# Kernel optimization log

Hardware: AMD Instinct MI355X
Metric: run time of the kernel (lower is better)

## Reference

```python
import jax, jax.numpy as jnp
import numpy as np

B, L, D, H = 2, 256, 128, 256


def silu_bwd(x):
    # NOTE: replicates the module's silu_backward exactly: silu(x) + sigmoid(x)*(1 - silu(x))
    s = jax.nn.silu(x)
    return s + jax.nn.sigmoid(x) * (1.0 - s)


def setup_inputs() -> dict:
    key = jax.random.key(0)
    ks = jax.random.split(key, 10)
    f32 = jnp.float32
    return {
        "x": jax.random.normal(ks[0], (B, L, D), f32),
        "W1_init": jax.random.normal(ks[1], (H, D), f32) * H ** -0.5,
        "b1_init": jnp.zeros((H,), f32),
        "W2_init": jax.random.normal(ks[2], (D, H), f32) * D ** -0.5,
        "b2_init": jnp.zeros((D,), f32),
        "Wq": jax.random.normal(ks[3], (D, D), f32) * D ** -0.5,
        "bq": jnp.zeros((D,), f32),
        "Wk": jax.random.normal(ks[4], (D, D), f32) * D ** -0.5,
        "bk": jnp.zeros((D,), f32),
        "Wv": jax.random.normal(ks[5], (D, D), f32) * D ** -0.5,
        "bv": jnp.zeros((D,), f32),
        "Wlr": jax.random.normal(ks[6], (1, D), f32) * D ** -0.5,
        "blr": jnp.zeros((1,), f32),
        "Wm": jax.random.normal(ks[7], (1, D), f32) * D ** -0.5,
        "bm": jnp.zeros((1,), f32),
        "Wwd": jax.random.normal(ks[8], (1, D), f32) * D ** -0.5,
        "bwd": jnp.zeros((1,), f32),
    }


def _forward(x, W1_init, b1_init, W2_init, b2_init, Wq, bq, Wk, bk, Wv, bv,
             Wlr, blr, Wm, bm, Wwd, bwd):
    b, l, d = x.shape
    q = x @ Wq.T + bq
    k = x @ Wk.T + bk
    v = x @ Wv.T + bv

    # fast-weight forward pass with initial weights (first call: state = init params)
    Z1 = jnp.einsum('hd,bld->blh', W1_init, k) + b1_init
    X2 = jax.nn.silu(Z1)
    Z2 = jnp.einsum('dh,blh->bld', W2_init, X2) + b2_init

    # per-token gradients of 0.5*||Z2 - v||^2
    gZ2 = Z2 - v
    gW2 = jnp.einsum('bld,blh->bldh', gZ2, X2)
    gX2 = jnp.einsum('bld,dh->blh', gZ2, W2_init)
    gZ1 = gX2 * silu_bwd(Z1)
    gW1 = jnp.einsum('blh,bld->blhd', gZ1, k)

    lr = jax.nn.softplus(x @ Wlr.T + blr)[..., 0]  # (b,l)
    gW1 = gW1 * lr[:, :, None, None]
    gb1 = gZ1 * lr[:, :, None]
    gW2 = gW2 * lr[:, :, None, None]
    gb2 = gZ2 * lr[:, :, None]

    strict = jnp.tril(jnp.ones((l, l), x.dtype), -1)  # row > col
    incl = jnp.tril(jnp.ones((l, l), x.dtype))        # row >= col

    # momentum: masked log-cumsum trick; [b,l,m] decay matrix
    log_mom = -jax.nn.softplus(-(x @ Wm.T + bm))[..., 0]  # (b,l)
    mom_cs = jnp.exp(jnp.cumsum(log_mom[:, :, None] * strict, axis=1)) * incl
    mW1 = jnp.einsum('blm,bmhd->blhd', mom_cs, gW1)
    mb1 = jnp.einsum('blm,bmh->blh', mom_cs, gb1)
    mW2 = jnp.einsum('blm,bmdh->bldh', mom_cs, gW2)
    mb2 = jnp.einsum('blm,bmd->bld', mom_cs, gb2)
    # cross-chunk momentum terms vanish (momentum state initialized to zero)

    # weight decay gating
    log_wd = -jax.nn.softplus(-(x @ Wwd.T + bwd))[..., 0]
    wd_cs = jnp.exp(jnp.cumsum(log_wd[:, :, None] * strict, axis=1)) * incl
    wd_full = jnp.exp(jnp.cumsum(log_wd, axis=1))  # (b,l)

    W1p = jnp.einsum('blm,bmhd->blhd', wd_cs, mW1) + wd_full[:, :, None, None] * W1_init
    b1p = jnp.einsum('blm,bmh->blh', wd_cs, mb1) + wd_full[:, :, None] * b1_init
    W2p = jnp.einsum('blm,bmdh->bldh', wd_cs, mW2) + wd_full[:, :, None, None] * W2_init
    b2p = jnp.einsum('blm,bmd->bld', wd_cs, mb2) + wd_full[:, :, None] * b2_init

    # query the per-token updated fast weights
    Zq1 = jnp.einsum('blhd,bld->blh', W1p, q) + b1p
    Xq2 = jax.nn.silu(Zq1)
    Zq2 = jnp.einsum('bldh,blh->bld', W2p, Xq2) + b2p
    return Zq2


def reference(x, W1_init, b1_init, W2_init, b2_init, Wq, bq, Wk, bk, Wv, bv,
              Wlr, blr, Wm, bm, Wwd, bwd):
    return _forward(x, W1_init, b1_init, W2_init, b2_init, Wq, bq, Wk, bk, Wv, bv,
                    Wlr, blr, Wm, bm, Wwd, bwd)
```

## Files before the change

### kernel.cpp

```cpp
#include <hip/hip_runtime.h>
#include <hip/hip_bf16.h>


#define Bc 2
#define Lc 256
#define Dc 128
#define Hc 256

__device__ __forceinline__ float sigf(float z)  { return 1.f / (1.f + expf(-z)); }
__device__ __forceinline__ float siluf(float z) { return z * sigf(z); }
__device__ __forceinline__ float silubwdf(float z) {
    float sg = sigf(z);
    float s  = z * sg;
    return s + sg * (1.f - s);
}
__device__ __forceinline__ float softplusf(float z) {
    if (z > 20.f)  return z;
    if (z < -20.f) return expf(z);
    return log1pf(expf(z));
}
__device__ __forceinline__ float dot4(float4 a, float4 b) {
    return a.x*b.x + a.y*b.y + a.z*b.z + a.w*b.w;
}

__global__ __launch_bounds__(256) void k_pre(
    const float* __restrict__ Wq, const float* __restrict__ Wk,
    const float* __restrict__ Wv, const float* __restrict__ W1,
    const float* __restrict__ W2,
    float4* __restrict__ Wq4, float4* __restrict__ Wk4, float4* __restrict__ Wv4,
    float4* __restrict__ W14, float4* __restrict__ W2q4, float4* __restrict__ W2c4)
{
    const int bb = blockIdx.x;
    if (bb < 112) {
        const float* in; float4* o; int M, N, base;
        if      (bb < 16) { in = Wq; o = Wq4;  M = 128; N = 128; base = 0;  }
        else if (bb < 32) { in = Wk; o = Wk4;  M = 128; N = 128; base = 16; }
        else if (bb < 48) { in = Wv; o = Wv4;  M = 128; N = 128; base = 32; }
        else if (bb < 80) { in = W1; o = W14;  M = 256; N = 128; base = 48; }
        else              { in = W2; o = W2q4; M = 128; N = 256; base = 80; }
        const int idx = (bb - base) * 256 + threadIdx.x;
        const int r = idx % M, g = idx / M;
        o[idx] = *(const float4*)(in + r * N + 4 * g);
    } else {
        const int idx = (bb - 112) * 256 + threadIdx.x;
        const int c = idx & 255, g = idx >> 8;
        W2c4[idx] = make_float4(W2[(4*g+0)*Hc + c], W2[(4*g+1)*Hc + c],
                                W2[(4*g+2)*Hc + c], W2[(4*g+3)*Hc + c]);
    }
}

__global__ __launch_bounds__(512, 4) void k_token(
    const float* __restrict__ x,
    const float* __restrict__ b1v, const float* __restrict__ b2v,
    const float* __restrict__ bq,  const float* __restrict__ bk,
    const float* __restrict__ bv,
    const float4* __restrict__ Wq4, const float4* __restrict__ Wk4,
    const float4* __restrict__ Wv4, const float4* __restrict__ W14,
    const float4* __restrict__ W2q4, const float4* __restrict__ W2c4,
    const float* __restrict__ Wlr, const float* __restrict__ blr,
    const float* __restrict__ Wm,  const float* __restrict__ bm,
    const float* __restrict__ Wwd, const float* __restrict__ bwd,
    float* __restrict__ qo, float* __restrict__ KT, float* __restrict__ X2T,
    float* __restrict__ z1q, float* __restrict__ GZ1, float* __restrict__ GZ2,
    float* __restrict__ Ssc, float* __restrict__ wdf)
{
    const int bb  = blockIdx.x;
    const int tid = threadIdx.x;

    if (bb >= Bc * Lc / 2) {
        __shared__ __align__(16) float lrS[Lc];
        __shared__ __align__(16) float lwS[Lc];
        __shared__ __align__(16) float ewdS[Lc];
        __shared__ __align__(16) float clmS[Lc];
        __shared__ __align__(16) float cwdS[Lc];
        const int b = bb - Bc * Lc / 2;
        const int l = tid;
        if (l < Lc) {
            const float4* xr4 = (const float4*)(x + (b * Lc + l) * Dc);
            const float4* wl4 = (const float4*)Wlr;
            const float4* wm4 = (const float4*)Wm;
            const float4* ww4 = (const float4*)Wwd;
            float dlr = blr[0], dm = bm[0], dw = bwd[0];
            #pragma unroll 4
            for (int j = 0; j < Dc / 4; ++j) {
                float4 xv = xr4[j];
                dlr += dot4(wl4[j], xv);
                dm  += dot4(wm4[j], xv);
                dw  += dot4(ww4[j], xv);
            }
            lrS[l] = softplusf(dlr);
            float lm = -softplusf(-dm);
            float lw = -softplusf(-dw);
            lwS[l]  = lw;
            clmS[l] = lm;
            cwdS[l] = lw;
        }
        __syncthreads();
        for (int off = 1; off < Lc; off <<= 1) {
            float a = 0.f, c = 0.f;
            if (l < Lc && l >= off) { a = clmS[l - off]; c = cwdS[l - off]; }
            __syncthreads();
            if (l < Lc) { clmS[l] += a; cwdS[l] += c; }
            __syncthreads();
        }
        if (l < Lc) {
            wdf[b * Lc + l] = expf(cwdS[l]);
            ewdS[l] = __expf(lwS[l]);
        }
        __syncthreads();
        if (l < Lc) {
            const int   m     = l;
            const float clm_m = clmS[m];
            const float lrm   = lrS[m];
            float* outp = Ssc + (b * Lc) * Lc + m;
            const int ll0 = m & ~63;
            {
                int zs = m - 3 < 0 ? 0 : m - 3;
                for (int ll = zs; ll < ll0; ++ll) outp[ll * Lc] = 0.f;
            }
            float s = 0.f;
            for (int ll4 = ll0; ll4 < Lc; ll4 += 8) {
                float4 cla = *(const float4*)&clmS[ll4];
                float4 clb = *(const float4*)&clmS[ll4 + 4];
                float4 ewa = *(const float4*)&ewdS[ll4];
                float4 ewb = *(const float4*)&ewdS[ll4 + 4];
                float ew[8] = {ewa.x, ewa.y, ewa.z, ewa.w,
                               ewb.x, ewb.y, ewb.z, ewb.w};
                float e2[8];
                e2[0] = __expf(cla.x - clm_m); e2[1] = __expf(cla.y - clm_m);
                e2[2] = __expf(cla.z - clm_m); e2[3] = __expf(cla.w - clm_m);
                e2[4] = __expf(clb.x - clm_m); e2[5] = __expf(clb.y - clm_m);
                e2[6] = __expf(clb.z - clm_m); e2[7] = __expf(clb.w - clm_m);
                #pragma unroll
                for (int u = 0; u < 8; ++u) {
                    const int ll = ll4 + u;
                    s = (ll >= m) ? (ew[u] * s + e2[u]) : 0.f;
                    outp[ll * Lc] = s * lrm;
                }
            }
        }
        return;
    }

    __shared__ __align__(16) float xs[2][Dc], qs[2][Dc], ks[2][Dc];
    __shared__ __align__(16) float X2s[2][Hc], z1s[2][Hc], gZ2s[2][Dc];
    __shared__ __align__(16) float pv[2][2][Dc], pz[4][2][Dc], pg[2][2][Hc];

    const int t0 = bb * 2;
    const int b  = t0 >> 8;
    const int l0 = t0 & 255;

    if (tid < 2 * Dc / 4)
        ((float4*)&xs[0][0])[tid] = ((const float4*)(x + t0 * Dc))[tid];
    __syncthreads();

    {
        const int g = tid >> 7, c = tid & 127;
        float4 wb[16];
        if (g < 2) {
            const float4* W = g ? Wk4 : Wq4;
            float a0 = (g ? bk : bq)[c], a1 = a0;
            for (int j4 = 0; j4 < 32; j4 += 16) {
                #pragma unroll
                for (int u = 0; u < 16; ++u) wb[u] = W[(j4+u) * Dc + c];
                #pragma unroll
                for (int u = 0; u < 16; ++u) {
                    a0 += dot4(wb[u], *(const float4*)&xs[0][4*(j4+u)]);
                    a1 += dot4(wb[u], *(const float4*)&xs[1][4*(j4+u)]);
                }
            }
            if (g == 0) {
                qs[0][c] = a0; qs[1][c] = a1;
                qo[t0 * Dc + c] = a0;
                qo[(t0 + 1) * Dc + c] = a1;
            } else {
                ks[0][c] = a0; ks[1][c] = a1;
                float* ktp = KT + (size_t)b * 32768;
                ktp[((c >> 2) * Lc + l0 + 0) * 4 + (c & 3)] = a0;
                ktp[((c >> 2) * Lc + l0 + 1) * 4 + (c & 3)] = a1;
            }
        } else {
            const int half = g - 2, j0 = half * 16;
            float av0 = 0.f, av1 = 0.f;
            #pragma unroll
            for (int u = 0; u < 16; ++u) wb[u] = Wv4[(j0+u) * Dc + c];
            #pragma unroll
            for (int u = 0; u < 16; ++u) {
                av0 += dot4(wb[u], *(const float4*)&xs[0][4*(j0+u)]);
                av1 += dot4(wb[u], *(const float4*)&xs[1][4*(j0+u)]);
            }
            pv[half][0][c] = av0; pv[half][1][c] = av1;
        }
    }
    __syncthreads();

    {
        const int which = tid >> 8, h = tid & 255;
        const float (*src)[Dc] = which ? qs : ks;
        float a0 = b1v[h], a1 = a0;
        float4 wb[16];
        for (int d4 = 0; d4 < 32; d4 += 16) {
            #pragma unroll
            for (int u = 0; u < 16; ++u) wb[u] = W14[(d4+u) * Hc + h];
            #pragma unroll
            for (int u = 0; u < 16; ++u) {
                a0 += dot4(wb[u], *(const float4*)&src[0][4*(d4+u)]);
                a1 += dot4(wb[u], *(const float4*)&src[1][4*(d4+u)]);
            }
        }
        if (which == 0) {
            z1s[0][h] = a0; z1s[1][h] = a1;
            float s0 = siluf(a0), s1 = siluf(a1);
            X2s[0][h] = s0; X2s[1][h] = s1;
            float* xtp = X2T + (size_t)b * 65536;
            xtp[((h >> 2) * Lc + l0 + 0) * 4 + (h & 3)] = s0;
            xtp[((h >> 2) * Lc + l0 + 1) * 4 + (h & 3)] = s1;
        } else {
            z1q[(t0 + 0) * Hc + h] = a0;
            z1q[(t0 + 1) * Hc + h] = a1;
        }
    }
    __syncthreads();

    {
        const int q4g = tid >> 7, d = tid & 127;
        const int h0 = q4g * 16;
        float a0 = 0.f, a1 = 0.f;
        float4 wb[16];
        #pragma unroll
        for (int u = 0; u < 16; ++u) wb[u] = W2q4[(h0+u) * Dc + d];
        #pragma unroll
        for (int u = 0; u < 16; ++u) {
            a0 += dot4(wb[u], *(const float4*)&X2s[0][4*(h0+u)]);
            a1 += dot4(wb[u], *(const float4*)&X2s[1][4*(h0+u)]);
        }
        pz[q4g][0][d] = a0; pz[q4g][1][d] = a1;
    }
    __syncthreads();
    if (tid < 2 * Dc) {
        const int t = tid >> 7, d = tid & 127;
        float g = pz[0][t][d] + pz[1][t][d] + pz[2][t][d] + pz[3][t][d] + b2v[d]
                - (pv[0][t][d] + pv[1][t][d] + bv[d]);
        gZ2s[t][d] = g;
        const int l = l0 + t;
        GZ2[(size_t)b * 32768 + ((l >> 2) * Dc + d) * 4 + (l & 3)] = g;
    }
    __syncthreads();

    {
        const int which = tid >> 8, h = tid & 255;
        const int d0 = which * 16;
        float a0 = 0.f, a1 = 0.f;
        float4 wb[16];
        #pragma unroll
        for (int u = 0; u < 16; ++u) wb[u] = W2c4[(d0+u) * Hc + h];
        #pragma unroll
        for (int u = 0; u < 16; ++u) {
            a0 += dot4(wb[u], *(const float4*)&gZ2s[0][4*(d0+u)]);
            a1 += dot4(wb[u], *(const float4*)&gZ2s[1][4*(d0+u)]);
        }
        pg[which][0][h] = a0; pg[which][1][h] = a1;
    }
    __syncthreads();
    {
        const int t = tid >> 8, h = tid & 255;
        const int l = l0 + t;
        GZ1[(size_t)b * 65536 + ((l >> 2) * Hc + h) * 4 + (l & 3)]
            = (pg[0][t][h] + pg[1][t][h]) * silubwdf(z1s[t][h]);
    }
}

__global__ __launch_bounds__(512, 4) void k_query(
    const float* __restrict__ qo,  const float* __restrict__ KT,
    const float* __restrict__ X2T, const float* __restrict__ GZ1,
    const float* __restrict__ GZ2, const float* __restrict__ z1q,
    const float* __restrict__ Ssc, const float* __restrict__ wdf,
    const float4* __restrict__ W2q4, const float* __restrict__ b2v,
    float* __restrict__ out)
{
    __shared__ __align__(16) float qs[2][Dc], ss[2][Lc], arow[2][Lc], xq2s[2][Hc];
    __shared__ __align__(16) float ps[2][2][Lc], pq[2][2][Hc];
    __shared__ __align__(16) float pm[4][2][Dc], pw[4][2][Dc];

    const int t0  = blockIdx.x * 2;
    const int b   = t0 >> 8;
    const int l0  = t0 & 255;
    const int tid = threadIdx.x;
    const int M4  = ((l0 + 1) >> 2) + 1;
    const int mPad = M4 * 4;

    if (tid < 2 * Dc / 4)
        ((float4*)&qs[0][0])[tid] = ((const float4*)(qo + t0 * Dc))[tid];
    if (tid < Lc) {
        ss[0][tid] = Ssc[(t0 + 0) * Lc + tid];
        ss[1][tid] = Ssc[(t0 + 1) * Lc + tid];
    }
    const float wdf0 = wdf[t0 + 0], wdf1 = wdf[t0 + 1];
    __syncthreads();

    {
        const int which = tid >> 8, m = tid & 255;
        if (m < mPad) {
            const float4* ktb = (const float4*)(KT + (size_t)b * 32768);
            const int d0 = which * 16;
            float acc0 = 0.f, acc1 = 0.f;
            float4 wb[16];
            #pragma unroll
            for (int u = 0; u < 16; ++u) wb[u] = ktb[(d0+u) * Lc + m];
            #pragma unroll
            for (int u = 0; u < 16; ++u) {
                acc0 += dot4(wb[u], *(const float4*)&qs[0][4*(d0+u)]);
                acc1 += dot4(wb[u], *(const float4*)&qs[1][4*(d0+u)]);
            }
            ps[which][0][m] = acc0; ps[which][1][m] = acc1;
        }
    }
    __syncthreads();
    {
        const int t = tid >> 8, m = tid & 255;
        if (m < mPad)
            arow[t][m] = ss[t][m] * (ps[0][t][m] + ps[1][t][m] + 1.f);
    }
    __syncthreads();

    {
        const int which = tid >> 8, h = tid & 255;
        const float4* g = (const float4*)(GZ1 + (size_t)b * 65536);
        const float4* ar0 = (const float4*)&arow[0][0];
        const float4* ar1 = (const float4*)&arow[1][0];
        float acc0 = 0.f, acc1 = 0.f;
        float4 wb[16];
        int m4 = which;
        for (; m4 + 30 < M4; m4 += 32) {
            #pragma unroll
            for (int u = 0; u < 16; ++u) wb[u] = g[(m4 + 2*u) * Hc + h];
            #pragma unroll
            for (int u = 0; u < 16; ++u) {
                acc0 += dot4(wb[u], ar0[m4 + 2*u]);
                acc1 += dot4(wb[u], ar1[m4 + 2*u]);
            }
        }
        for (; m4 < M4; m4 += 2) {
            float4 gv = g[m4 * Hc + h];
            acc0 += dot4(gv, ar0[m4]);
            acc1 += dot4(gv, ar1[m4]);
        }
        pq[which][0][h] = acc0; pq[which][1][h] = acc1;
    }
    __syncthreads();
    {
        const int t = tid >> 8, h = tid & 255;
        const float w = t ? wdf1 : wdf0;
        xq2s[t][h] = siluf(pq[0][t][h] + pq[1][t][h]
                           + w * z1q[(t0 + t) * Hc + h]);
    }
    __syncthreads();

    {
        const int which = tid >> 8, m = tid & 255;
        if (m < mPad) {
            const float4* xtb = (const float4*)(X2T + (size_t)b * 65536);
            const int h0 = which * 32;
            float acc0 = 0.f, acc1 = 0.f;
            float4 wb[16];
            for (int h4 = h0; h4 < h0 + 32; h4 += 16) {
                #pragma unroll
                for (int u = 0; u < 16; ++u) wb[u] = xtb[(h4+u) * Lc + m];
                #pragma unroll
                for (int u = 0; u < 16; ++u) {
                    acc0 += dot4(wb[u], *(const float4*)&xq2s[0][4*(h4+u)]);
                    acc1 += dot4(wb[u], *(const float4*)&xq2s[1][4*(h4+u)]);
                }
            }
            ps[which][0][m] = acc0; ps[which][1][m] = acc1;
        }
    }
    __syncthreads();
    {
        const int t = tid >> 8, m = tid & 255;
        if (m < mPad)
            arow[t][m] = ss[t][m] * (ps[0][t][m] + ps[1][t][m] + 1.f);
    }
    __syncthreads();

    {
        const int q4g = tid >> 7, d = tid & 127;
        const float4* g2  = (const float4*)(GZ2 + (size_t)b * 32768);
        const float4* ar0 = (const float4*)&arow[0][0];
        const float4* ar1 = (const float4*)&arow[1][0];
        float am0 = 0.f, am1 = 0.f, aw0 = 0.f, aw1 = 0.f;
        float4 wb[16];
        int m4 = q4g;
        for (; m4 + 60 < M4; m4 += 64) {
            #pragma unroll
            for (int u = 0; u < 16; ++u) wb[u] = g2[(m4 + 4*u) * Dc + d];
            #pragma unroll
            for (int u = 0; u < 16; ++u) {
                am0 += dot4(wb[u], ar0[m4 + 4*u]);
                am1 += dot4(wb[u], ar1[m4 + 4*u]);
            }
        }
        for (; m4 < M4; m4 += 4) {
            float4 gv = g2[m4 * Dc + d];
            am0 += dot4(gv, ar0[m4]);
            am1 += dot4(gv, ar1[m4]);
        }
        const int h0 = q4g * 16;
        #pragma unroll
        for (int u = 0; u < 16; ++u) wb[u] = W2q4[(h0+u) * Dc + d];
        #pragma unroll
        for (int u = 0; u < 16; ++u) {
            aw0 += dot4(wb[u], *(const float4*)&xq2s[0][4*(h0+u)]);
            aw1 += dot4(wb[u], *(const float4*)&xq2s[1][4*(h0+u)]);
        }
        pm[q4g][0][d] = am0; pm[q4g][1][d] = am1;
        pw[q4g][0][d] = aw0; pw[q4g][1][d] = aw1;
    }
    __syncthreads();
    if (tid < 2 * Dc) {
        const int t = tid >> 7, d = tid & 127;
        const float w = t ? wdf1 : wdf0;
        out[(t0 + t) * Dc + d] =
            (pm[0][t][d] + pm[1][t][d] + pm[2][t][d] + pm[3][t][d])
            + w * (b2v[d] + pw[0][t][d] + pw[1][t][d] + pw[2][t][d] + pw[3][t][d]);
    }
}

extern "C" void kernel_launch(void* const* d_in, const int* in_sizes, int n_in,
                              void* d_out, int out_size, void* d_ws, size_t ws_size,
                              hipStream_t stream)
{
    const float* x   = (const float*)d_in[0];
    const float* W1  = (const float*)d_in[1];
    const float* b1  = (const float*)d_in[2];
    const float* W2  = (const float*)d_in[3];
    const float* b2  = (const float*)d_in[4];
    const float* Wq  = (const float*)d_in[5];
    const float* bq  = (const float*)d_in[6];
    const float* Wk  = (const float*)d_in[7];
    const float* bk  = (const float*)d_in[8];
    const float* Wv  = (const float*)d_in[9];
    const float* bv  = (const float*)d_in[10];
    const float* Wlr = (const float*)d_in[11];
    const float* blr = (const float*)d_in[12];
    const float* Wm  = (const float*)d_in[13];
    const float* bm  = (const float*)d_in[14];
    const float* Wwd = (const float*)d_in[15];
    const float* bwd = (const float*)d_in[16];

    float* ws = (float*)d_ws;
    float*  qo   = ws;
    float*  KT   = ws + 65536;
    float*  X2T  = ws + 131072;
    float*  GZ1  = ws + 262144;
    float*  GZ2  = ws + 393216;
    float*  z1q  = ws + 458752;
    float*  Ssc  = ws + 589824;
    float*  wdf  = ws + 720896;
    float4* Wq4  = (float4*)(ws + 721408);
    float4* Wk4  = (float4*)(ws + 737792);
    float4* Wv4  = (float4*)(ws + 754176);
    float4* W14  = (float4*)(ws + 770560);
    float4* W2q4 = (float4*)(ws + 803328);
    float4* W2c4 = (float4*)(ws + 836096);
    float*  out  = (float*)d_out;

    k_pre<<<144, 256, 0, stream>>>(Wq, Wk, Wv, W1, W2,
                                   Wq4, Wk4, Wv4, W14, W2q4, W2c4);
    k_token<<<Bc * Lc / 2 + Bc, 512, 0, stream>>>(x, b1, b2, bq, bk, bv,
                                                  Wq4, Wk4, Wv4, W14, W2q4, W2c4,
                                                  Wlr, blr, Wm, bm, Wwd, bwd,
                                                  qo, KT, X2T, z1q, GZ1, GZ2,
                                                  Ssc, wdf);
    k_query<<<Bc * Lc / 2, 512, 0, stream>>>(qo, KT, X2T, GZ1, GZ2, z1q,
                                             Ssc, wdf, W2q4, b2, out);
}
```

Before: 126.0 us.

## Double block size to 1024 threads and split dot-product reductions further

Both k_token and k_query now launch 1024 threads per block instead of 512. Each matrix-vector phase is divided into more partial-sum groups with shorter inner loops and smaller register tiles (8 float4 instead of 16 in several places), reduced through new shared-memory partial buffers. The V projection is now reduced separately into a shared vs buffer. The aim is to shorten each thread's serial dependency chain and hide more memory latency in these latency-bound, per-token kernels. The cost is extra reduction steps, more shared memory, and tighter register limits from the larger launch bound, with possible spills. The unseen special-block branch for bb >= 256 must also be correct with 1024 threads.

```diff
diff --git a/kernel.cpp b/kernel.cpp
--- a/kernel.cpp
+++ b/kernel.cpp
@@ -49,7 +49,7 @@
     }
 }
 
-__global__ __launch_bounds__(512, 4) void k_token(
+__global__ __launch_bounds__(1024, 4) void k_token(
     const float* __restrict__ x,
     const float* __restrict__ b1v, const float* __restrict__ b2v,
     const float* __restrict__ bq,  const float* __restrict__ bk,
@@ -142,9 +142,13 @@
         return;
     }
 
-    __shared__ __align__(16) float xs[2][Dc], qs[2][Dc], ks[2][Dc];
+    __shared__ __align__(16) float xs[2][Dc], qs[2][Dc], ks[2][Dc], vs[2][Dc];
     __shared__ __align__(16) float X2s[2][Hc], z1s[2][Hc], gZ2s[2][Dc];
-    __shared__ __align__(16) float pv[2][2][Dc], pz[4][2][Dc], pg[2][2][Hc];
+    __shared__ __align__(16) float pqk[4][2][Dc];
+    __shared__ __align__(16) float pv4[4][2][Dc];
+    __shared__ __align__(16) float p2[4][2][Hc];
+    __shared__ __align__(16) float pz8[8][2][Dc];
+    __shared__ __align__(16) float pg4[4][2][Hc];
 
     const int t0 = bb * 2;
     const int b  = t0 >> 8;
@@ -156,91 +160,103 @@
 
     {
         const int g = tid >> 7, c = tid & 127;
-        float4 wb[16];
-        if (g < 2) {
-            const float4* W = g ? Wk4 : Wq4;
-            float a0 = (g ? bk : bq)[c], a1 = a0;
-            for (int j4 = 0; j4 < 32; j4 += 16) {
-                #pragma unroll
-                for (int u = 0; u < 16; ++u) wb[u] = W[(j4+u) * Dc + c];
-                #pragma unroll
-                for (int u = 0; u < 16; ++u) {
-                    a0 += dot4(wb[u], *(const float4*)&xs[0][4*(j4+u)]);
-                    a1 += dot4(wb[u], *(const float4*)&xs[1][4*(j4+u)]);
-                }
-            }
-            if (g == 0) {
-                qs[0][c] = a0; qs[1][c] = a1;
-                qo[t0 * Dc + c] = a0;
-                qo[(t0 + 1) * Dc + c] = a1;
-            } else {
-                ks[0][c] = a0; ks[1][c] = a1;
-                float* ktp = KT + (size_t)b * 32768;
-                ktp[((c >> 2) * Lc + l0 + 0) * 4 + (c & 3)] = a0;
-                ktp[((c >> 2) * Lc + l0 + 1) * 4 + (c & 3)] = a1;
-            }
+        if (g < 4) {
+            const int isK = g >> 1, dh = g & 1;
+            const float4* W = isK ? Wk4 : Wq4;
+            const int j0 = dh * 16;
+            float a0 = 0.f, a1 = 0.f;
+            float4 wb[16];
+            #pragma unroll
+            for (int u = 0; u < 16; ++u) wb[u] = W[(j0+u) * Dc + c];
+            #pragma unroll
+            for (int u = 0; u < 16; ++u) {
+                a0 += dot4(wb[u], *(const float4*)&xs[0][4*(j0+u)]);
+                a1 += dot4(wb[u], *(const float4*)&xs[1][4*(j0+u)]);
+            }
+            pqk[g][0][c] = a0; pqk[g][1][c] = a1;
         } else {
-            const int half = g - 2, j0 = half * 16;
-            float av0 = 0.f, av1 = 0.f;
-            #pragma unroll
-            for (int u = 0; u < 16; ++u) wb[u] = Wv4[(j0+u) * Dc + c];
-            #pragma unroll
-            for (int u = 0; u < 16; ++u) {
-                av0 += dot4(wb[u], *(const float4*)&xs[0][4*(j0+u)]);
-                av1 += dot4(wb[u], *(const float4*)&xs[1][4*(j0+u)]);
-            }
-            pv[half][0][c] = av0; pv[half][1][c] = av1;
-        }
+            const int qtr = g - 4, j0 = qtr * 8;
+            float a0 = 0.f, a1 = 0.f;
+            float4 wb[8];
+            #pragma unroll
+            for (int u = 0; u < 8; ++u) wb[u] = Wv4[(j0+u) * Dc + c];
+            #pragma unroll
+            for (int u = 0; u < 8; ++u) {
+                a0 += dot4(wb[u], *(const float4*)&xs[0][4*(j0+u)]);
+                a1 += dot4(wb[u], *(const float4*)&xs[1][4*(j0+u)]);
+            }
+            pv4[qtr][0][c] = a0; pv4[qtr][1][c] = a1;
+        }
+    }
+    __syncthreads();
+    if (tid < 256) {
+        const int t = tid >> 7, c = tid & 127;
+        float v = pqk[0][t][c] + pqk[1][t][c] + bq[c];
+        qs[t][c] = v;
+        qo[(t0 + t) * Dc + c] = v;
+    } else if (tid < 512) {
+        const int i = tid - 256, t = i >> 7, c = i & 127;
+        float v = pqk[2][t][c] + pqk[3][t][c] + bk[c];
+        ks[t][c] = v;
+        KT[(size_t)b * 32768 + ((c >> 2) * Lc + l0 + t) * 4 + (c & 3)] = v;
+    } else if (tid < 768) {
+        const int i = tid - 512, t = i >> 7, c = i & 127;
+        vs[t][c] = pv4[0][t][c] + pv4[1][t][c] + pv4[2][t][c]
+                 + pv4[3][t][c] + bv[c];
     }
     __syncthreads();
 
     {
         const int which = tid >> 8, h = tid & 255;
-        const float (*src)[Dc] = which ? qs : ks;
-        float a0 = b1v[h], a1 = a0;
-        float4 wb[16];
-        for (int d4 = 0; d4 < 32; d4 += 16) {
-            #pragma unroll
-            for (int u = 0; u < 16; ++u) wb[u] = W14[(d4+u) * Hc + h];
-            #pragma unroll
-            for (int u = 0; u < 16; ++u) {
-                a0 += dot4(wb[u], *(const float4*)&src[0][4*(d4+u)]);
-                a1 += dot4(wb[u], *(const float4*)&src[1][4*(d4+u)]);
-            }
-        }
-        if (which == 0) {
-            z1s[0][h] = a0; z1s[1][h] = a1;
-            float s0 = siluf(a0), s1 = siluf(a1);
-            X2s[0][h] = s0; X2s[1][h] = s1;
-            float* xtp = X2T + (size_t)b * 65536;
-            xtp[((h >> 2) * Lc + l0 + 0) * 4 + (h & 3)] = s0;
-            xtp[((h >> 2) * Lc + l0 + 1) * 4 + (h & 3)] = s1;
-        } else {
-            z1q[(t0 + 0) * Hc + h] = a0;
-            z1q[(t0 + 1) * Hc + h] = a1;
-        }
-    }
-    __syncthreads();
-
-    {
-        const int q4g = tid >> 7, d = tid & 127;
-        const int h0 = q4g * 16;
+        const int srcq = which & 1, dh = which >> 1;
+        const float (*src)[Dc] = srcq ? qs : ks;
+        const int d0 = dh * 16;
         float a0 = 0.f, a1 = 0.f;
         float4 wb[16];
         #pragma unroll
-        for (int u = 0; u < 16; ++u) wb[u] = W2q4[(h0+u) * Dc + d];
+        for (int u = 0; u < 16; ++u) wb[u] = W14[(d0+u) * Hc + h];
         #pragma unroll
         for (int u = 0; u < 16; ++u) {
+            a0 += dot4(wb[u], *(const float4*)&src[0][4*(d0+u)]);
+            a1 += dot4(wb[u], *(const float4*)&src[1][4*(d0+u)]);
+        }
+        p2[which][0][h] = a0; p2[which][1][h] = a1;
+    }
+    __syncthreads();
+    {
+        const int sel = tid >> 9, i = tid & 511, t = i >> 8, h = i & 255;
+        if (sel == 0) {
+            float z = p2[0][t][h] + p2[2][t][h] + b1v[h];
+            z1s[t][h] = z;
+            float s = siluf(z);
+            X2s[t][h] = s;
+            X2T[(size_t)b * 65536 + ((h >> 2) * Lc + l0 + t) * 4 + (h & 3)] = s;
+        } else {
+            z1q[(t0 + t) * Hc + h] = p2[1][t][h] + p2[3][t][h] + b1v[h];
+        }
+    }
+    __syncthreads();
+
+    {
+        const int g = tid >> 7, d = tid & 127;
+        const int h0 = g * 8;
+        float a0 = 0.f, a1 = 0.f;
+        float4 wb[8];
+        #pragma unroll
+        for (int u = 0; u < 8; ++u) wb[u] = W2q4[(h0+u) * Dc + d];
+        #pragma unroll
+        for (int u = 0; u < 8; ++u) {
             a0 += dot4(wb[u], *(const float4*)&X2s[0][4*(h0+u)]);
             a1 += dot4(wb[u], *(const float4*)&X2s[1][4*(h0+u)]);
         }
-        pz[q4g][0][d] = a0; pz[q4g][1][d] = a1;
-    }
-    __syncthreads();
-    if (tid < 2 * Dc) {
+        pz8[g][0][d] = a0; pz8[g][1][d] = a1;
+    }
+    __syncthreads();
+    if (tid < 256) {
         const int t = tid >> 7, d = tid & 127;
-        float g = pz[0][t][d] + pz[1][t][d] + pz[2][t][d] + pz[3][t][d] + b2v[d]
-                - (pv[0][t][d] + pv[1][t][d] + bv[d]);
+        float g = pz8[0][t][d] + pz8[1][t][d] + pz8[2][t][d] + pz8[3][t][d]
+                + pz8[4][t][d] + pz8[5][t][d] + pz8[6][t][d] + pz8[7][t][d]
+                + b2v[d] - vs[t][d];
         gZ2s[t][d] = g;
         const int l = l0 + t;
         GZ2[(size_t)b * 32768 + ((l >> 2) * Dc + d) * 4 + (l & 3)] = g;
@@ -248,29 +264,30 @@
     __syncthreads();
 
     {
-        const int which = tid >> 8, h = tid & 255;
-        const int d0 = which * 16;
+        const int g = tid >> 8, h = tid & 255;
+        const int d0 = g * 8;
         float a0 = 0.f, a1 = 0.f;
-        float4 wb[16];
+        float4 wb[8];
         #pragma unroll
-        for (int u = 0; u < 16; ++u) wb[u] = W2c4[(d0+u) * Hc + h];
+        for (int u = 0; u < 8; ++u) wb[u] = W2c4[(d0+u) * Hc + h];
         #pragma unroll
-        for (int u = 0; u < 16; ++u) {
+        for (int u = 0; u < 8; ++u) {
             a0 += dot4(wb[u], *(const float4*)&gZ2s[0][4*(d0+u)]);
             a1 += dot4(wb[u], *(const float4*)&gZ2s[1][4*(d0+u)]);
         }
-        pg[which][0][h] = a0; pg[which][1][h] = a1;
-    }
-    __syncthreads();
-    {
+        pg4[g][0][h] = a0; pg4[g][1][h] = a1;
+    }
+    __syncthreads();
+    if (tid < 512) {
         const int t = tid >> 8, h = tid & 255;
         const int l = l0 + t;
+        float a = pg4[0][t][h] + pg4[1][t][h] + pg4[2][t][h] + pg4[3][t][h];
         GZ1[(size_t)b * 65536 + ((l >> 2) * Hc + h) * 4 + (l & 3)]
-            = (pg[0][t][h] + pg[1][t][h]) * silubwdf(z1s[t][h]);
-    }
-}
-
-__global__ __launch_bounds__(512, 4) void k_query(
+            = a * silubwdf(z1s[t][h]);
+    }
+}
+
+__global__ __launch_bounds__(1024, 4) void k_query(
     const float* __restrict__ qo,  const float* __restrict__ KT,
     const float* __restrict__ X2T, const float* __restrict__ GZ1,
     const float* __restrict__ GZ2, const float* __restrict__ z1q,
@@ -279,8 +296,9 @@
     float* __restrict__ out)
 {
     __shared__ __align__(16) float qs[2][Dc], ss[2][Lc], arow[2][Lc], xq2s[2][Hc];
-    __shared__ __align__(16) float ps[2][2][Lc], pq[2][2][Hc];
-    __shared__ __align__(16) float pm[4][2][Dc], pw[4][2][Dc];
+    __shared__ __align__(16) float psc[4][2][Lc];
+    __shared__ __align__(16) float pzq[4][2][Hc];
+    __shared__ __align__(16) float pm4[4][2][Dc], pw4[4][2][Dc];
 
     const int t0  = blockIdx.x * 2;
     const int b   = t0 >> 8;
@@ -291,9 +309,9 @@
 
     if (tid < 2 * Dc / 4)
         ((float4*)&qs[0][0])[tid] = ((const float4*)(qo + t0 * Dc))[tid];
-    if (tid < Lc) {
-        ss[0][tid] = Ssc[(t0 + 0) * Lc + tid];
-        ss[1][tid] = Ssc[(t0 + 1) * Lc + tid];
+    if (tid >= 512 && tid < 1024) {
+        const int i = tid - 512, t = i >> 8, m = i & 255;
+        ss[t][m] = Ssc[(t0 + t) * Lc + m];
     }
     const float wdf0 = wdf[t0 + 0], wdf1 = wdf[t0 + 1];
     __syncthreads();
@@ -302,24 +320,25 @@
         const int which = tid >> 8, m = tid & 255;
         if (m < mPad) {
             const float4* ktb = (const float4*)(KT + (size_t)b * 32768);
-            const int d0 = which * 16;
+            const int d0 = which * 8;
             float acc0 = 0.f, acc1 = 0.f;
-            float4 wb[16];
-            #pragma unroll
-            for (int u = 0; u < 16; ++u) wb[u] = ktb[(d0+u) * Lc + m];
-            #pragma unroll
-            for (int u = 0; u < 16; ++u) {
+            float4 wb[8];
+            #pragma unroll
+            for (int u = 0; u < 8; ++u) wb[u] = ktb[(d0+u) * Lc + m];
+            #pragma unroll
+            for (int u = 0; u < 8; ++u) {
                 acc0 += dot4(wb[u], *(const float4*)&qs[0][4*(d0+u)]);
                 acc1 += dot4(wb[u], *(const float4*)&qs[1][4*(d0+u)]);
             }
-            ps[which][0][m] = acc0; ps[which][1][m] = acc1;
-        }
-    }
-    __syncthreads();
-    {
+            psc[which][0][m] = acc0; psc[which][1][m] = acc1;
+        }
+    }
+    __syncthreads();
+    if (tid < 512) {
         const int t = tid >> 8, m = tid & 255;
         if (m < mPad)
-            arow[t][m] = ss[t][m] * (ps[0][t][m] + ps[1][t][m] + 1.f);
+            arow[t][m] = ss[t][m] * (psc[0][t][m] + psc[1][t][m]
+                                   + psc[2][t][m] + psc[3][t][m] + 1.f);
     }
     __syncthreads();
 
@@ -331,28 +350,28 @@
         float acc0 = 0.f, acc1 = 0.f;
         float4 wb[16];
         int m4 = which;
-        for (; m4 + 30 < M4; m4 += 32) {
-            #pragma unroll
-            for (int u = 0; u < 16; ++u) wb[u] = g[(m4 + 2*u) * Hc + h];
+        for (; m4 + 60 < M4; m4 += 64) {
+            #pragma unroll
+            for (int u = 0; u < 16; ++u) wb[u] = g[(m4 + 4*u) * Hc + h];
             #pragma unroll
             for (int u = 0; u < 16; ++u) {
-                acc0 += dot4(wb[u], ar0[m4 + 2*u]);
-                acc1 += dot4(wb[u], ar1[m4 + 2*u]);
-            }
-        }
-        for (; m4 < M4; m4 += 2) {
+                acc0 += dot4(wb[u], ar0[m4 + 4*u]);
+                acc1 += dot4(wb[u], ar1[m4 + 4*u]);
+            }
+        }
+        for (; m4 < M4; m4 += 4) {
             float4 gv = g[m4 * Hc + h];
             acc0 += dot4(gv, ar0[m4]);
             acc1 += dot4(gv, ar1[m4]);
         }
-        pq[which][0][h] = acc0; pq[which][1][h] = acc1;
-    }
-    __syncthreads();
-    {
+        pzq[which][0][h] = acc0; pzq[which][1][h] = acc1;
+    }
+    __syncthreads();
+    if (tid < 512) {
         const int t = tid >> 8, h = tid & 255;
         const float w = t ? wdf1 : wdf0;
-        xq2s[t][h] = siluf(pq[0][t][h] + pq[1][t][h]
-                           + w * z1q[(t0 + t) * Hc + h]);
+        xq2s[t][h] = siluf(pzq[0][t][h] + pzq[1][t][h] + pzq[2][t][h]
+                           + pzq[3][t][h] + w * z1q[(t0 + t) * Hc + h]);
     }
     __syncthreads();
 
@@ -360,69 +379,74 @@
         const int which = tid >> 8, m = tid & 255;
         if (m < mPad) {
             const float4* xtb = (const float4*)(X2T + (size_t)b * 65536);
-            const int h0 = which * 32;
+            const int h0 = which * 16;
             float acc0 = 0.f, acc1 = 0.f;
             float4 wb[16];
-            for (int h4 = h0; h4 < h0 + 32; h4 += 16) {
+            #pragma unroll
+            for (int u = 0; u < 16; ++u) wb[u] = xtb[(h0+u) * Lc + m];
+            #pragma unroll
+            for (int u = 0; u < 16; ++u) {
+                acc0 += dot4(wb[u], *(const float4*)&xq2s[0][4*(h0+u)]);
+                acc1 += dot4(wb[u], *(const float4*)&xq2s[1][4*(h0+u)]);
+            }
+            psc[which][0][m] = acc0; psc[which][1][m] = acc1;
+        }
+    }
+    __syncthreads();
+    if (tid < 512) {
+        const int t = tid >> 8, m = tid & 255;
+        if (m < mPad)
+            arow[t][m] = ss[t][m] * (psc[0][t][m] + psc[1][t][m]
+                                   + psc[2][t][m] + psc[3][t][m] + 1.f);
+    }
+    __syncthreads();
+
+    {
+        const int g8 = tid >> 7, d = tid & 127;
+        if (g8 < 4) {
+            const float4* g2  = (const float4*)(GZ2 + (size_t)b * 32768);
+            const float4* ar0 = (const float4*)&arow[0][0];
+            const float4* ar1 = (const float4*)&arow[1][0];
+            float am0 = 0.f, am1 = 0.f;
+            float4 wb[16];
+            int m4 = g8;
+            for (; m4 + 60 < M4; m4 += 64) {
                 #pragma unroll
-                for (int u = 0; u < 16; ++u) wb[u] = xtb[(h4+u) * Lc + m];
+                for (int u = 0; u < 16; ++u) wb[u] = g2[(m4 + 4*u) * Dc + d];
                 #pragma unroll
                 for (int u = 0; u < 16; ++u) {
-                    acc0 += dot4(wb[u], *(const float4*)&xq2s[0][4*(h4+u)]);
-                    acc1 += dot4(wb[u], *(const float4*)&xq2s[1][4*(h4+u)]);
+                    am0 += dot4(wb[u], ar0[m4 + 4*u]);
+                    am1 += dot4(wb[u], ar1[m4 + 4*u]);
                 }
             }
-            ps[which][0][m] = acc0; ps[which][1][m] = acc1;
-        }
-    }
-    __syncthreads();
-    {
-        const int t = tid >> 8, m = tid & 255;
-        if (m < mPad)
-            arow[t][m] = ss[t][m] * (ps[0][t][m] + ps[1][t][m] + 1.f);
-    }
-    __syncthreads();
-
-    {
-        const int q4g = tid >> 7, d = tid & 127;
-        const float4* g2  = (const float4*)(GZ2 + (size_t)b * 32768);
-        const float4* ar0 = (const float4*)&arow[0][0];
-        const float4* ar1 = (const float4*)&arow[1][0];
-        float am0 = 0.f, am1 = 0.f, aw0 = 0.f, aw1 = 0.f;
-        float4 wb[16];
-        int m4 = q4g;
-        for (; m4 + 60 < M4; m4 += 64) {
-            #pragma unroll
-            for (int u = 0; u < 16; ++u) wb[u] = g2[(m4 + 4*u) * Dc + d];
+            for (; m4 < M4; m4 += 4) {
+                float4 gv = g2[m4 * Dc + d];
+                am0 += dot4(gv, ar0[m4]);
+                am1 += dot4(gv, ar1[m4]);
+            }
+            pm4[g8][0][d] = am0; pm4[g8][1][d] = am1;
+        } else {
+            const int h0 = (g8 - 4) * 16;
+            float aw0 = 0.f, aw1 = 0.f;
+            float4 wb[16];
+            #pragma unroll
+            for (int u = 0; u < 16; ++u) wb[u] = W2q4[(h0+u) * Dc + d];
             #pragma unroll
             for (int u = 0; u < 16; ++u) {
-                am0 += dot4(wb[u], ar0[m4 + 4*u]);
-                am1 += dot4(wb[u], ar1[m4 + 4*u]);
-            }
-        }
-        for (; m4 < M4; m4 += 4) {
-            float4 gv = g2[m4 * Dc + d];
-            am0 += dot4(gv, ar0[m4]);
-            am1 += dot4(gv, ar1[m4]);
-        }
-        const int h0 = q4g * 16;
-        #pragma unroll
-        for (int u = 0; u < 16; ++u) wb[u] = W2q4[(h0+u) * Dc + d];
-        #pragma unroll
-        for (int u = 0; u < 16; ++u) {
-            aw0 += dot4(wb[u], *(const float4*)&xq2s[0][4*(h0+u)]);
-            aw1 += dot4(wb[u], *(const float4*)&xq2s[1][4*(h0+u)]);
-        }
-        pm[q4g][0][d] = am0; pm[q4g][1][d] = am1;
-        pw[q4g][0][d] = aw0; pw[q4g][1][d] = aw1;
+                aw0 += dot4(wb[u], *(const float4*)&xq2s[0][4*(h0+u)]);
+                aw1 += dot4(wb[u], *(const float4*)&xq2s[1][4*(h0+u)]);
+            }
+            pw4[g8 - 4][0][d] = aw0; pw4[g8 - 4][1][d] = aw1;
+        }
     }
     __syncthreads();
     if (tid < 2 * Dc) {
         const int t = tid >> 7, d = tid & 127;
         const float w = t ? wdf1 : wdf0;
         out[(t0 + t) * Dc + d] =
-            (pm[0][t][d] + pm[1][t][d] + pm[2][t][d] + pm[3][t][d])
-            + w * (b2v[d] + pw[0][t][d] + pw[1][t][d] + pw[2][t][d] + pw[3][t][d]);
+            (pm4[0][t][d] + pm4[1][t][d] + pm4[2][t][d] + pm4[3][t][d])
+            + w * (b2v[d] + pw4[0][t][d] + pw4[1][t][d]
+                          + pw4[2][t][d] + pw4[3][t][d]);
     }
 }
 
@@ -467,11 +491,11 @@
 
     k_pre<<<144, 256, 0, stream>>>(Wq, Wk, Wv, W1, W2,
                                    Wq4, Wk4, Wv4, W14, W2q4, W2c4);
-    k_token<<<Bc * Lc / 2 + Bc, 512, 0, stream>>>(x, b1, b2, bq, bk, bv,
-                                                  Wq4, Wk4, Wv4, W14, W2q4, W2c4,
-                                                  Wlr, blr, Wm, bm, Wwd, bwd,
-                                                  qo, KT, X2T, z1q, GZ1, GZ2,
-                                                  Ssc, wdf);
-    k_query<<<Bc * Lc / 2, 512, 0, stream>>>(qo, KT, X2T, GZ1, GZ2, z1q,
-                                             Ssc, wdf, W2q4, b2, out);
-}
+    k_token<<<Bc * Lc / 2 + Bc, 1024, 0, stream>>>(x, b1, b2, bq, bk, bv,
+                                                   Wq4, Wk4, Wv4, W14, W2q4, W2c4,
+                                                   Wlr, blr, Wm, bm, Wwd, bwd,
+                                                   qo, KT, X2T, z1q, GZ1, GZ2,
+                                                   Ssc, wdf);
+    k_query<<<Bc * Lc / 2, 1024, 0, stream>>>(qo, KT, X2T, GZ1, GZ2, z1q,
+                                              Ssc, wdf, W2q4, b2, out);
+}
```

Measured after the change: 127.8 us. About the same (+1.5%).
